# Kernel tuning notes

Measured on AMD Instinct MI355X. Metric: run time of the kernel, lower is better.

Reference implementation:

```python
import jax, jax.numpy as jnp
import numpy as np

ALPHA = 0.5
EPS_COS = 1e-6
EPS_PNORM = 1e-7


def _heuristic_importance(edge_index, num_nodes):
    # n_imp = row-sum of D^-1 (A + I) D^-1, then sqrt (LADIES-style importance).
    row, col = edge_index[0], edge_index[1]
    ones = jnp.ones(row.shape[0], dtype=jnp.float32)
    deg = jax.ops.segment_sum(ones, row, num_segments=num_nodes) + 1.0  # +1 self loop
    deg_inv = jnp.where(deg > 0, 1.0 / deg, 0.0)
    nbr_sum = jax.ops.segment_sum(deg_inv[col], row, num_segments=num_nodes)
    s = deg_inv * (nbr_sum + deg_inv)  # self-loop term deg_inv[i]*deg_inv[i]
    return jnp.sqrt(jnp.maximum(s, 0.0))


def _cosine(a, b):
    # torch CosineSimilarity(dim=-1, eps=1e-6)
    dot = jnp.sum(a * b, axis=-1)
    na = jnp.maximum(jnp.linalg.norm(a, axis=-1), EPS_COS)
    nb = jnp.maximum(jnp.linalg.norm(b, axis=-1), EPS_COS)
    return dot / (na * nb)


def setup_inputs() -> dict:
    key = jax.random.key(0)
    ks = jax.random.split(key, 8)
    N, F, B, K, E = 500000, 128, 1024, 256, 4000000
    return {
        "x": jax.random.normal(ks[0], (N, F), dtype=jnp.float32),
        "w_ego_root": jax.random.normal(ks[1], (F,), dtype=jnp.float32) / np.sqrt(F),
        "w_ego_u": jax.random.normal(ks[2], (F,), dtype=jnp.float32) / np.sqrt(F),
        "w_layer_v": jax.random.normal(ks[3], (F, 1), dtype=jnp.float32) / np.sqrt(F),
        "w_layer_u": jax.random.normal(ks[4], (F, 1), dtype=jnp.float32) / np.sqrt(F),
        "roots": jax.random.randint(ks[5], (B,), 0, N, dtype=jnp.int32),
        "neighbors": jax.random.randint(ks[6], (B, K), 0, N, dtype=jnp.int32),
        "edge_index": jax.random.randint(ks[7], (2, E), 0, N, dtype=jnp.int32),
    }


def reference(x, w_ego_root, w_ego_u, w_layer_v, w_layer_u, roots, neighbors, edge_index):
    N = x.shape[0]
    n_imp = _heuristic_importance(edge_index, N)       # [N]

    x_root = x[roots]                                   # [B, F]  gather
    x_u = x[neighbors]                                  # [B, K, F] gather (dominant traffic)

    # ego kernel: cosine(h_root * w_ego_root, h_u * w_ego_u)
    h_root = x_root * w_ego_root                        # [B, F]
    h_u = x_u * w_ego_u                                 # [B, K, F]
    ego_score = _cosine(h_root[:, None, :], h_u)        # [B, K]

    # layer kernel: msg from root v to every sampled u, relu, L2-normalize over u dim
    h_v = (x_root @ w_layer_v)                          # [B, 1]
    h_ul = (x_u @ w_layer_u)[..., 0]                    # [B, K]
    pre = jax.nn.relu(h_v + h_ul)                       # [B, K]
    norm = jnp.maximum(jnp.linalg.norm(pre, axis=1, keepdims=True), 1e-12)
    layer_score = pre / norm                            # [B, K]

    p_u = (ALPHA * ego_score + (1.0 - ALPHA) * layer_score) * n_imp[neighbors]
    p_norm = jax.lax.stop_gradient(p_u[:, 0])           # hop-1 norm (cloned/detached)
    p_u = p_u / (p_norm[:, None] + EPS_PNORM) + 1.0
    p_clip = jnp.clip(p_u, 0.01, 1.0)
    w = p_clip * (p_u > 0)                              # keep-mask (expected multinomial weight)

    # probability-weighted aggregation of sampled neighbor features
    out = jnp.einsum("bk,bkf->bf", w, x_u)              # [B, F]
    return out
```

## Files before the change

kernel.cpp:

```cpp
#include <hip/hip_runtime.h>
#include <hip/hip_bf16.h>

constexpr int F = 128;
constexpr int K = 256;
constexpr float FXSCALE = 8388608.0f;
constexpr float FXINV   = 1.0f / 8388608.0f;

constexpr int NFIX = 500000;
constexpr int EFIX = 4000000;

constexpr int SLB  = 13;
constexpr int SLSZ = 8192;
constexpr int NSL  = 62;
constexpr int PB   = 250;
constexpr int PCE  = EFIX / PB;
constexpr int CH   = 5;
constexpr int PBC  = PB / CH;
constexpr int SCAP = 352;
constexpr int WD   = SLSZ / 2;
constexpr int NTILE = NSL * CH;


__global__ __launch_bounds__(512) void partition_kernel(const int* __restrict__ row,
                                                        const int* __restrict__ col,
                                                        unsigned* __restrict__ counts,
                                                        unsigned* __restrict__ pedges) {
    __shared__ unsigned cnt[NSL];
    const int bid = blockIdx.x, t = threadIdx.x;
    if (t < NSL) cnt[t] = 0;
    __syncthreads();

    const int beg = bid * PCE;
    const int end = beg + PCE;
    for (int i = beg + t * 4; i + 4 <= end; i += 512 * 4) {
        int4 r  = *(const int4*)(row + i);
        int4 cl = *(const int4*)(col + i);
        {
            unsigned rr = (unsigned)r.x, s = rr >> SLB;
            unsigned off = atomicAdd(&cnt[s], 1u);
            if (off < (unsigned)SCAP)
                pedges[((size_t)s * PB + bid) * SCAP + off] = ((unsigned)cl.x << SLB) | (rr & (SLSZ - 1));
        }
        {
            unsigned rr = (unsigned)r.y, s = rr >> SLB;
            unsigned off = atomicAdd(&cnt[s], 1u);
            if (off < (unsigned)SCAP)
                pedges[((size_t)s * PB + bid) * SCAP + off] = ((unsigned)cl.y << SLB) | (rr & (SLSZ - 1));
        }
        {
            unsigned rr = (unsigned)r.z, s = rr >> SLB;
            unsigned off = atomicAdd(&cnt[s], 1u);
            if (off < (unsigned)SCAP)
                pedges[((size_t)s * PB + bid) * SCAP + off] = ((unsigned)cl.z << SLB) | (rr & (SLSZ - 1));
        }
        {
            unsigned rr = (unsigned)r.w, s = rr >> SLB;
            unsigned off = atomicAdd(&cnt[s], 1u);
            if (off < (unsigned)SCAP)
                pedges[((size_t)s * PB + bid) * SCAP + off] = ((unsigned)cl.w << SLB) | (rr & (SLSZ - 1));
        }
    }
    __syncthreads();
    if (t < NSL) counts[t * PB + bid] = min(cnt[t], (unsigned)SCAP);
}

__global__ __launch_bounds__(1024) void deg_hist2_kernel(const unsigned* __restrict__ pedges,
                                                         const unsigned* __restrict__ counts,
                                                         unsigned* __restrict__ parts) {
    __shared__ unsigned hist[WD];
    __shared__ unsigned ccnt[PBC];
    const int tile = blockIdx.x;
    const int s = tile / CH, c = tile % CH;
    const int t = threadIdx.x;
    for (int w = t; w < WD; w += 1024) hist[w] = 0;
    if (t < PBC) ccnt[t] = counts[s * PB + c * PBC + t];
    __syncthreads();
    const unsigned* src = pedges + ((size_t)s * PB + (size_t)c * PBC) * SCAP;
    for (int idx = t; idx < PBC * SCAP; idx += 1024) {
        int bb = idx / SCAP;
        int i  = idx - bb * SCAP;
        if ((unsigned)i < ccnt[bb]) {
            unsigned rl = src[idx] & (SLSZ - 1);
            atomicAdd(&hist[rl >> 1], 1u << ((rl & 1) * 16));
        }
    }
    __syncthreads();
    unsigned* dst = parts + (size_t)tile * WD;
    for (int w = t; w < WD; w += 1024) dst[w] = hist[w];
}

__global__ void degq_reduce2_kernel(const unsigned* __restrict__ parts,
                                    unsigned* __restrict__ degq) {
    int gw = blockIdx.x * blockDim.x + threadIdx.x;
    if (gw >= NSL * WD) return;
    int s = gw >> 12, w = gw & (WD - 1);
    const unsigned* p = parts + (size_t)s * CH * WD + w;
    unsigned acc = 0;
    #pragma unroll
    for (int c = 0; c < CH; ++c) acc += p[(size_t)c * WD];
    int n0 = (s << SLB) + (w << 1);
    float i0 = 1.0f / (float)((acc & 0xffffu) + 1u);
    float i1 = 1.0f / (float)((acc >> 16) + 1u);
    unsigned q0 = (unsigned)(i0 * FXSCALE + 0.5f);
    unsigned q1 = (unsigned)(i1 * FXSCALE + 0.5f);
    if (n0 + 1 < NFIX)      *(uint2*)(degq + n0) = make_uint2(q0, q1);
    else if (n0 < NFIX)     degq[n0] = q0;
}

__global__ __launch_bounds__(1024) void nbr_hist2_kernel(const unsigned* __restrict__ pedges,
                                                         const unsigned* __restrict__ counts,
                                                         const unsigned* __restrict__ degq,
                                                         unsigned* __restrict__ parts) {
    __shared__ unsigned hist[SLSZ];
    __shared__ unsigned ccnt[PBC];
    const int tile = blockIdx.x;
    const int s = tile / CH, c = tile % CH;
    const int t = threadIdx.x;
    for (int w = t; w < SLSZ; w += 1024) hist[w] = 0;
    if (t < PBC) ccnt[t] = counts[s * PB + c * PBC + t];
    __syncthreads();
    const unsigned* src = pedges + ((size_t)s * PB + (size_t)c * PBC) * SCAP;
    for (int idx = t; idx < PBC * SCAP; idx += 1024) {
        int bb = idx / SCAP;
        int i  = idx - bb * SCAP;
        if ((unsigned)i < ccnt[bb]) {
            unsigned pe = src[idx];
            atomicAdd(&hist[pe & (SLSZ - 1)], degq[pe >> SLB]);
        }
    }
    __syncthreads();
    unsigned* dst = parts + (size_t)tile * SLSZ;
    for (int w = t; w < SLSZ; w += 1024) dst[w] = hist[w];
}

__global__ void nimp_reduce2_kernel(const unsigned* __restrict__ parts,
                                    const unsigned* __restrict__ degq,
                                    float* __restrict__ nimp) {
    int i = blockIdx.x * blockDim.x + threadIdx.x;
    if (i >= NFIX) return;
    int s = i >> SLB, rl = i & (SLSZ - 1);
    const unsigned* p = parts + (size_t)s * CH * SLSZ + rl;
    unsigned acc = 0;
    #pragma unroll
    for (int c = 0; c < CH; ++c) acc += p[(size_t)c * SLSZ];
    float dinv = (float)degq[i] * FXINV;
    float nbr  = (float)acc * FXINV;
    nimp[i] = sqrtf(fmaxf(dinv * (nbr + dinv), 0.0f));
}


__global__ void zero_kernel(int* p, int n) {
    int i = blockIdx.x * blockDim.x + threadIdx.x;
    if (i < n) p[i] = 0;
}

__global__ void deg_kernel(const int* __restrict__ row, int E, int* cnt) {
    int e = blockIdx.x * blockDim.x + threadIdx.x;
    if (e < E) atomicAdd(&cnt[row[e]], 1);
}

__global__ void deginv_kernel(int* buf, int N) {
    int i = blockIdx.x * blockDim.x + threadIdx.x;
    if (i < N) {
        int c = buf[i];
        ((float*)buf)[i] = 1.0f / (float)(c + 1);
    }
}

__global__ void nbrsum_kernel(const int* __restrict__ row, const int* __restrict__ col,
                              int E, const float* __restrict__ deg_inv, float* nbr_sum) {
    int e = blockIdx.x * blockDim.x + threadIdx.x;
    if (e < E) unsafeAtomicAdd(&nbr_sum[row[e]], deg_inv[col[e]]);
}

__global__ void nimp_kernel(const float* __restrict__ deg_inv, float* buf, int N) {
    int i = blockIdx.x * blockDim.x + threadIdx.x;
    if (i < N) {
        float dinv = deg_inv[i];
        float s = dinv * (buf[i] + dinv);
        buf[i] = sqrtf(fmaxf(s, 0.0f));
    }
}


__global__ __launch_bounds__(512, 8) void sampler_main(
    const float* __restrict__ x,
    const float* __restrict__ w_ego_root,
    const float* __restrict__ w_ego_u,
    const float* __restrict__ w_layer_v,
    const float* __restrict__ w_layer_u,
    const int* __restrict__ roots,
    const int* __restrict__ neighbors,
    const float* __restrict__ nimp,
    float* __restrict__ out)
{
    __shared__ __align__(16) float g_s[F];
    __shared__ __align__(16) float weu_s[F];
    __shared__ __align__(16) float wlu_s[F];
    __shared__ float d_p[2][K];
    __shared__ float n_p[2][K];
    __shared__ float h_p[2][K];
    __shared__ float ego_s[K];
    __shared__ float pre_s[K];
    __shared__ float praw_s[K];
    __shared__ float wgt_s[K];
    __shared__ float part_s[8][F];
    __shared__ float scal_s[4];
    __shared__ int   nbr_s[K];

    const int b = blockIdx.x;
    const int t = threadIdx.x;
    const int root = roots[b];
    const int* nbr = neighbors + (size_t)b * K;

    float ni = 0.0f;
    if (t < K) {
        int mn = nbr[t];
        nbr_s[t] = mn;
        ni = nimp[mn];
    }
    if (t < F) {
        float xr  = x[(size_t)root * F + t];
        float hr  = xr * w_ego_root[t];
        float wu  = w_ego_u[t];
        g_s[t]   = hr * wu;
        weu_s[t] = wu;
        wlu_s[t] = w_layer_u[t];
        ego_s[t] = hr * hr;
        pre_s[t] = xr * w_layer_v[t];
    }
    __syncthreads();

    if (t < 64) {
        float a = ego_s[t] + ego_s[t + 64];
        float h = pre_s[t] + pre_s[t + 64];
        for (int m = 1; m < 64; m <<= 1) {
            a += __shfl_xor(a, m);
            h += __shfl_xor(h, m);
        }
        if (t == 0) {
            scal_s[0] = fmaxf(sqrtf(a), 1e-6f);
            scal_s[1] = h;
        }
    }
    __syncthreads();

    const int k  = t & (K - 1);
    const int hh = t >> 8;

    {
        const float* rowp = x + (size_t)nbr_s[k] * F + hh * 64;
        const float4* gp = (const float4*)(g_s + hh * 64);
        const float4* ep = (const float4*)(weu_s + hh * 64);
        const float4* lp = (const float4*)(wlu_s + hh * 64);
        float d = 0.0f, nb2 = 0.0f, hu = 0.0f;
        #pragma unroll 16
        for (int f4 = 0; f4 < 16; ++f4) {
            float4 v  = ((const float4*)rowp)[f4];
            float4 g  = gp[f4];
            float4 eu = ep[f4];
            float4 lu = lp[f4];
            d   += g.x * v.x + g.y * v.y + g.z * v.z + g.w * v.w;
            float u0 = v.x * eu.x, u1 = v.y * eu.y, u2 = v.z * eu.z, u3 = v.w * eu.w;
            nb2 += u0 * u0 + u1 * u1 + u2 * u2 + u3 * u3;
            hu  += lu.x * v.x + lu.y * v.y + lu.z * v.z + lu.w * v.w;
        }
        d_p[hh][k] = d;
        n_p[hh][k] = nb2;
        h_p[hh][k] = hu;
    }
    __syncthreads();

    if (t < K) {
        float d   = d_p[0][t] + d_p[1][t];
        float nb2 = n_p[0][t] + n_p[1][t];
        float hu  = h_p[0][t] + h_p[1][t];
        float nb  = fmaxf(sqrtf(nb2), 1e-6f);
        ego_s[t] = d / (scal_s[0] * nb);
        pre_s[t] = fmaxf(scal_s[1] + hu, 0.0f);
    }
    __syncthreads();

    if (t < 64) {
        float s = 0.0f;
        for (int kk = t; kk < K; kk += 64) s += pre_s[kk] * pre_s[kk];
        for (int m = 1; m < 64; m <<= 1) s += __shfl_xor(s, m);
        if (t == 0) scal_s[2] = fmaxf(sqrtf(s), 1e-12f);
    }
    __syncthreads();

    if (t < K) {
        float layer = pre_s[t] / scal_s[2];
        praw_s[t] = (0.5f * ego_s[t] + 0.5f * layer) * ni;
    }
    __syncthreads();

    if (t < K) {
        float pn = praw_s[0] + 1e-7f;
        float pu = praw_s[t] / pn + 1.0f;
        float pc = fminf(fmaxf(pu, 0.01f), 1.0f);
        wgt_s[t] = (pu > 0.0f) ? pc : 0.0f;
    }
    __syncthreads();

    const int wave = t >> 6;
    const int lane = t & 63;
    {
        float ax = 0.0f, ay = 0.0f;
        #pragma unroll 4
        for (int kk = wave; kk < K; kk += 8) {
            float2 v = ((const float2*)(x + (size_t)nbr_s[kk] * F))[lane];
            float w = wgt_s[kk];
            ax += w * v.x;
            ay += w * v.y;
        }
        ((float2*)part_s[wave])[lane] = make_float2(ax, ay);
    }
    __syncthreads();

    if (t < F) {
        float r = 0.0f;
        #pragma unroll
        for (int g = 0; g < 8; ++g) r += part_s[g][t];
        out[(size_t)b * F + t] = r;
    }
}


extern "C" void kernel_launch(void* const* d_in, const int* in_sizes, int n_in,
                              void* d_out, int out_size, void* d_ws, size_t ws_size,
                              hipStream_t stream) {
    const float* x    = (const float*)d_in[0];
    const float* werr = (const float*)d_in[1];
    const float* weu  = (const float*)d_in[2];
    const float* wlv  = (const float*)d_in[3];
    const float* wlu  = (const float*)d_in[4];
    const int*   roots = (const int*)d_in[5];
    const int*   nbrs  = (const int*)d_in[6];
    const int*   eidx  = (const int*)d_in[7];

    const int N = in_sizes[0] / F;
    const int B = in_sizes[5];
    const int E = in_sizes[7] / 2;
    const int* erow = eidx;
    const int* ecol = eidx + E;

    float* out = (float*)d_out;
    const int TB = 256;

    const size_t PEDGES_W = (size_t)NSL * PB * SCAP;
    const size_t PARTS_W  = (size_t)NTILE * SLSZ;
    const size_t CNT_W    = (size_t)NSL * PB;
    size_t need_fast = (PEDGES_W + PARTS_W + NFIX + NFIX + CNT_W) * 4;

    if (N == NFIX && E == EFIX && ws_size >= need_fast) {
        unsigned* pedges = (unsigned*)d_ws;
        unsigned* parts  = pedges + PEDGES_W;
        unsigned* degq   = parts + PARTS_W;
        float*    nimp   = (float*)(degq + NFIX);
        unsigned* counts = (unsigned*)(nimp + NFIX);

        partition_kernel<<<PB, 512, 0, stream>>>(erow, ecol, counts, pedges);
        deg_hist2_kernel<<<NTILE, 1024, 0, stream>>>(pedges, counts, parts);
        degq_reduce2_kernel<<<(NSL * WD + TB - 1) / TB, TB, 0, stream>>>(parts, degq);
        nbr_hist2_kernel<<<NTILE, 1024, 0, stream>>>(pedges, counts, degq, parts);
        nimp_reduce2_kernel<<<(NFIX + TB - 1) / TB, TB, 0, stream>>>(parts, degq, nimp);
        sampler_main<<<B, 512, 0, stream>>>(x, werr, weu, wlv, wlu, roots, nbrs,
                                            nimp, out);
    } else {
        float* buf0 = (float*)d_ws;
        float* buf1 = buf0 + N;

        zero_kernel<<<(2 * N + TB - 1) / TB, TB, 0, stream>>>((int*)buf0, 2 * N);
        deg_kernel<<<(E + TB - 1) / TB, TB, 0, stream>>>(erow, E, (int*)buf0);
        deginv_kernel<<<(N + TB - 1) / TB, TB, 0, stream>>>((int*)buf0, N);
        nbrsum_kernel<<<(E + TB - 1) / TB, TB, 0, stream>>>(erow, ecol, E, buf0, buf1);
        nimp_kernel<<<(N + TB - 1) / TB, TB, 0, stream>>>(buf0, buf1, N);
        sampler_main<<<B, 512, 0, stream>>>(x, werr, weu, wlv, wlu, roots, nbrs,
                                            buf1, out);
    }
}
```

Measured before the change: 115.3 us.

## Stage gathered neighbor rows in LDS as fp16 and reuse them for aggregation

During the scoring pass each thread now writes its gathered neighbor row into a shared-memory tile stored as half precision. The final weighted aggregation reads from that tile instead of gathering the same rows from global memory a second time, which removes the repeated 256x128 float gather per root. Scratch arrays are aliased into one union buffer to save LDS, and the launch-bounds occupancy hint drops from 8 to 4. The cost is roughly 66 KB of LDS per block, which lowers occupancy, plus fp16 rounding of the aggregated features that may loosen accuracy against the fp32 reference.

```diff
diff --git a/kernel.cpp b/kernel.cpp
--- a/kernel.cpp
+++ b/kernel.cpp
@@ -1,5 +1,6 @@
 #include <hip/hip_runtime.h>
 #include <hip/hip_bf16.h>
+#include <hip/hip_fp16.h>
 
 constexpr int F = 128;
 constexpr int K = 256;
@@ -183,7 +184,7 @@
 }
 
 
-__global__ __launch_bounds__(512, 8) void sampler_main(
+__global__ __launch_bounds__(512, 4) void sampler_main(
     const float* __restrict__ x,
     const float* __restrict__ w_ego_root,
     const float* __restrict__ w_ego_u,
@@ -197,16 +198,19 @@
     __shared__ __align__(16) float g_s[F];
     __shared__ __align__(16) float weu_s[F];
     __shared__ __align__(16) float wlu_s[F];
-    __shared__ float d_p[2][K];
-    __shared__ float n_p[2][K];
-    __shared__ float h_p[2][K];
     __shared__ float ego_s[K];
     __shared__ float pre_s[K];
     __shared__ float praw_s[K];
     __shared__ float wgt_s[K];
-    __shared__ float part_s[8][F];
     __shared__ float scal_s[4];
     __shared__ int   nbr_s[K];
+    __shared__ float ubuf[6 * K];
+    __shared__ __half tile[K][130];
+
+    float* d_p = ubuf;
+    float* n_p = ubuf + 2 * K;
+    float* h_p = ubuf + 4 * K;
+    float* part = ubuf;
 
     const int b = blockIdx.x;
     const int t = threadIdx.x;
@@ -253,6 +257,7 @@
         const float4* gp = (const float4*)(g_s + hh * 64);
         const float4* ep = (const float4*)(weu_s + hh * 64);
         const float4* lp = (const float4*)(wlu_s + hh * 64);
+        __half* trow = &tile[k][hh * 64];
         float d = 0.0f, nb2 = 0.0f, hu = 0.0f;
         #pragma unroll 16
         for (int f4 = 0; f4 < 16; ++f4) {
@@ -264,17 +269,19 @@
             float u0 = v.x * eu.x, u1 = v.y * eu.y, u2 = v.z * eu.z, u3 = v.w * eu.w;
             nb2 += u0 * u0 + u1 * u1 + u2 * u2 + u3 * u3;
             hu  += lu.x * v.x + lu.y * v.y + lu.z * v.z + lu.w * v.w;
-        }
-        d_p[hh][k] = d;
-        n_p[hh][k] = nb2;
-        h_p[hh][k] = hu;
+            ((__half2*)(trow + f4 * 4))[0] = __floats2half2_rn(v.x, v.y);
+            ((__half2*)(trow + f4 * 4))[1] = __floats2half2_rn(v.z, v.w);
+        }
+        d_p[hh * K + k] = d;
+        n_p[hh * K + k] = nb2;
+        h_p[hh * K + k] = hu;
     }
     __syncthreads();
 
     if (t < K) {
-        float d   = d_p[0][t] + d_p[1][t];
-        float nb2 = n_p[0][t] + n_p[1][t];
-        float hu  = h_p[0][t] + h_p[1][t];
+        float d   = d_p[t] + d_p[K + t];
+        float nb2 = n_p[t] + n_p[K + t];
+        float hu  = h_p[t] + h_p[K + t];
         float nb  = fmaxf(sqrtf(nb2), 1e-6f);
         ego_s[t] = d / (scal_s[0] * nb);
         pre_s[t] = fmaxf(scal_s[1] + hu, 0.0f);
@@ -307,21 +314,22 @@
     const int lane = t & 63;
     {
         float ax = 0.0f, ay = 0.0f;
-        #pragma unroll 4
-        for (int kk = wave; kk < K; kk += 8) {
-            float2 v = ((const float2*)(x + (size_t)nbr_s[kk] * F))[lane];
+        const int k0 = wave * 32;
+        #pragma unroll 8
+        for (int kk = k0; kk < k0 + 32; ++kk) {
             float w = wgt_s[kk];
+            float2 v = __half22float2(*(const __half2*)&tile[kk][2 * lane]);
             ax += w * v.x;
             ay += w * v.y;
         }
-        ((float2*)part_s[wave])[lane] = make_float2(ax, ay);
+        ((float2*)(part + wave * F))[lane] = make_float2(ax, ay);
     }
     __syncthreads();
 
     if (t < F) {
         float r = 0.0f;
         #pragma unroll
-        for (int g = 0; g < 8; ++g) r += part_s[g][t];
+        for (int g = 0; g < 8; ++g) r += part[g * F + t];
         out[(size_t)b * F + t] = r;
     }
 }
```

New measurement: 98.45 us. 1.17x faster.
